# Kernel tuning notes

Measured on AMD Instinct MI355X. Metric: run time of the kernel, lower is better.

Reference implementation:

```python
import jax, jax.numpy as jnp
import numpy as np

N_NODES = 100000
N_EDGES = 1600000
IN_DIM = 128
OUT_DIM = 128
N_HEADS = 4


def setup_inputs() -> dict:
    key = jax.random.key(0)
    k1, k2, k3, k4, k5 = jax.random.split(key, 5)
    h = jax.random.normal(k1, (N_NODES, IN_DIM), dtype=jnp.float32)
    src = jax.random.randint(k2, (N_EDGES,), 0, N_NODES, dtype=jnp.int32)
    dst = jax.random.randint(k3, (N_EDGES,), 0, N_NODES, dtype=jnp.int32)
    s = 1.0 / np.sqrt(IN_DIM)
    W_self = jax.random.normal(k4, (N_HEADS, IN_DIM, OUT_DIM), dtype=jnp.float32) * s
    W_neigh = jax.random.normal(k5, (N_HEADS, IN_DIM, OUT_DIM), dtype=jnp.float32) * s
    b = jnp.zeros((N_HEADS, OUT_DIM), dtype=jnp.float32)
    return {"h": h, "src": src, "dst": dst, "W_self": W_self, "W_neigh": W_neigh, "b": b}


def reference(h, src, dst, W_self, W_neigh, b):
    # Mean neighbor aggregation (shared across heads: SAGEConv 'mean' aggregates
    # raw features, then applies per-head linear layers).
    neigh_sum = jax.ops.segment_sum(h[src], dst, num_segments=N_NODES)   # [N, d_in]
    deg = jax.ops.segment_sum(jnp.ones_like(src, dtype=h.dtype), dst,
                              num_segments=N_NODES)                      # [N]
    h_neigh = neigh_sum / jnp.maximum(deg, 1.0)[:, None]                  # [N, d_in]

    # Per-head: fc_self(h_dst) + fc_neigh(h_neigh) + bias -> [H, N, d_out]
    out = (jnp.einsum('nd,hdo->hno', h, W_self)
           + jnp.einsum('nd,hdo->hno', h_neigh, W_neigh)
           + b[:, None, :])
    # merge='mean': average heads
    return jnp.mean(out, axis=0)  # [N, d_out]
```

## Files before the change

kernel.cpp:

```cpp
#include <hip/hip_runtime.h>

#define N_NODES 100000
#define N_EDGES 1600000
#define DIM 128
#define NH 4

#define NPB 512
#define NB 196
#define CAP 12288
#define BCHUNK 8192
#define BEPT 32
#define NBLK ((N_EDGES + BCHUNK - 1) / BCHUNK)

typedef __attribute__((ext_vector_type(8))) short bf16x8;
typedef __attribute__((ext_vector_type(4))) float f32x4;
typedef __attribute__((ext_vector_type(8))) unsigned short u16x8;

#define B_BCUR   0u
#define B_ROWOFF 4096u
#define B_BBASE  404096u
#define B_CSR    405504u
#define B_WPACK  6805504u
#define B_BAVG   6871040u
#define B_HB     6871552u
#define NEED_BF16 32869376ull

__device__ inline unsigned short f2bf(float x) {
    union { float f; unsigned u; } v; v.f = x;
    unsigned r = v.u + 0x7fffu + ((v.u >> 16) & 1u);
    return (unsigned short)(r >> 16);
}

template <bool BF>
__global__ __launch_bounds__(256) void prep_kernel(
    const float* __restrict__ h, unsigned short* __restrict__ hb,
    const float* __restrict__ Ws, const float* __restrict__ Wn,
    const float* __restrict__ b, unsigned short* __restrict__ wpack,
    float* __restrict__ bavg, int* __restrict__ bcur) {
    const int t = threadIdx.x;
    if (blockIdx.x == 0) bcur[t] = t * CAP;
    int i = blockIdx.x * 256 + t;
    if (i < DIM * DIM) {
        float s = 0.f, n = 0.f;
#pragma unroll
        for (int hh = 0; hh < NH; ++hh) {
            s += Ws[hh * DIM * DIM + i];
            n += Wn[hh * DIM * DIM + i];
        }
        s *= 0.25f; n *= 0.25f;
        int k = i >> 7, o = i & 127;
        int nt = o >> 4, lanelo = o & 15;
        int ks = k >> 5, lanehi = (k & 31) >> 3, e = k & 7;
        int pos = (((nt * 4 + ks) * 64) + lanehi * 16 + lanelo) * 8 + e;
        wpack[pos] = f2bf(s);
        wpack[16384 + pos] = f2bf(n);
    }
    if (i < DIM) {
        float bb = 0.f;
#pragma unroll
        for (int hh = 0; hh < NH; ++hh) bb += b[hh * DIM + i];
        bavg[i] = 0.25f * bb;
    }
    if (BF) {
        const float4* p = reinterpret_cast<const float4*>(h) + (size_t)i * 2;
        float4 a = p[0], c = p[1];
        u16x8 r;
        r[0] = f2bf(a.x); r[1] = f2bf(a.y); r[2] = f2bf(a.z); r[3] = f2bf(a.w);
        r[4] = f2bf(c.x); r[5] = f2bf(c.y); r[6] = f2bf(c.z); r[7] = f2bf(c.w);
        reinterpret_cast<u16x8*>(hb)[i] = r;
    }
}

__global__ __launch_bounds__(256) void bucket_scatter_kernel(const int* __restrict__ src,
                                                             const int* __restrict__ dst,
                                                             int* __restrict__ bcur,
                                                             int* __restrict__ ebuf) {
    __shared__ int stage[BCHUNK];
    __shared__ unsigned char bkt[BCHUNK];
    __shared__ int lc[256], lbase[256], lpos[256];
    int t = threadIdx.x;
    lc[t] = 0;
    lpos[t] = 0;
    __syncthreads();
    int e0 = blockIdx.x * BCHUNK;
#pragma unroll 4
    for (int j = 0; j < BEPT; ++j) {
        int e = e0 + j * 256 + t;
        if (e < N_EDGES) {
            int d = dst[e];
            stage[j * 256 + t] = (src[e] << 9) | (d & (NPB - 1));
            bkt[j * 256 + t] = (unsigned char)(d >> 9);
            atomicAdd(&lc[d >> 9], 1);
        }
    }
    __syncthreads();
    if (lc[t]) lbase[t] = atomicAdd(&bcur[t], lc[t]);
    __syncthreads();
#pragma unroll 4
    for (int j = 0; j < BEPT; ++j) {
        int e = e0 + j * 256 + t;
        if (e < N_EDGES) {
            int bb = bkt[j * 256 + t];
            int o = atomicAdd(&lpos[bb], 1);
            ebuf[lbase[bb] + o] = stage[j * 256 + t];
        }
    }
}

__global__ __launch_bounds__(256) void bucket_scan_kernel(const int* __restrict__ bcur,
                                                          int* __restrict__ bbase) {
    __shared__ int s[256];
    int t = threadIdx.x;
    int v = bcur[t] - t * CAP;
    s[t] = v;
    __syncthreads();
    for (int off = 1; off < 256; off <<= 1) {
        int add = (t >= off) ? s[t - off] : 0;
        __syncthreads();
        s[t] += add;
        __syncthreads();
    }
    bbase[t] = s[t] - v;
}

__global__ __launch_bounds__(256) void csr_build_kernel(const int* __restrict__ bcur,
                                                        const int* __restrict__ bbase,
                                                        const int* __restrict__ ebuf,
                                                        int* __restrict__ rowoff,
                                                        int* __restrict__ csr) {
    __shared__ int h[NPB], off[NPB], cur[NPB], ss[256];
    int b = blockIdx.x, t = threadIdx.x;
    int cnt = bcur[b] - b * CAP;
    int ibase = b * CAP;
    int obase = bbase[b];
    h[t] = 0; h[t + 256] = 0;
    cur[t] = 0; cur[t + 256] = 0;
    __syncthreads();
    for (int i = t; i < cnt; i += 256) atomicAdd(&h[ebuf[ibase + i] & (NPB - 1)], 1);
    __syncthreads();
    int e0 = h[2 * t], e1 = h[2 * t + 1];
    ss[t] = e0 + e1;
    __syncthreads();
    for (int o = 1; o < 256; o <<= 1) {
        int add = (t >= o) ? ss[t - o] : 0;
        __syncthreads();
        ss[t] += add;
        __syncthreads();
    }
    int ex = ss[t] - (e0 + e1);
    off[2 * t] = ex;
    off[2 * t + 1] = ex + e0;
    __syncthreads();
    int n0 = b * NPB;
#pragma unroll
    for (int k = 0; k < 2; ++k) {
        int s2 = 2 * t + k;
        int n = n0 + s2;
        int dg = (k == 0) ? e0 : e1;
        if (n < N_NODES) rowoff[n] = ((obase + off[s2]) << 9) | min(dg, 511);
    }
    for (int i = t; i < cnt; i += 256) {
        int p = ebuf[ibase + i];
        int nl = p & (NPB - 1);
        int o = atomicAdd(&cur[nl], 1);
        csr[obase + off[nl] + o] = p >> 9;
    }
}

template <bool BF>
__global__ __launch_bounds__(256) void gather_mean_kernel(
    const float* __restrict__ h, const unsigned short* __restrict__ hb,
    const int* __restrict__ rowoff, const int* __restrict__ csr,
    float* __restrict__ out) {
    int node = blockIdx.x * 4 + (threadIdx.x >> 6);
    int lane = threadIdx.x & 63;
    int g = lane >> 4;
    int c = lane & 15;
    int w = rowoff[node];
    int lo = w >> 9;
    int dg = w & 511;
    int hi = lo + dg;
    float a0 = 0.f, a1 = 0.f, a2 = 0.f, a3 = 0.f;
    float a4 = 0.f, a5 = 0.f, a6 = 0.f, a7 = 0.f;
    if (BF) {
        int k = lo + g;
        for (; k + 4 < hi; k += 8) {
            int s0 = csr[k], s1 = csr[k + 4];
            uint4 v = *reinterpret_cast<const uint4*>(hb + (size_t)s0 * DIM + c * 8);
            uint4 ww = *reinterpret_cast<const uint4*>(hb + (size_t)s1 * DIM + c * 8);
            a0 += __uint_as_float(v.x << 16) + __uint_as_float(ww.x << 16);
            a1 += __uint_as_float(v.x & 0xffff0000u) + __uint_as_float(ww.x & 0xffff0000u);
            a2 += __uint_as_float(v.y << 16) + __uint_as_float(ww.y << 16);
            a3 += __uint_as_float(v.y & 0xffff0000u) + __uint_as_float(ww.y & 0xffff0000u);
            a4 += __uint_as_float(v.z << 16) + __uint_as_float(ww.z << 16);
            a5 += __uint_as_float(v.z & 0xffff0000u) + __uint_as_float(ww.z & 0xffff0000u);
            a6 += __uint_as_float(v.w << 16) + __uint_as_float(ww.w << 16);
            a7 += __uint_as_float(v.w & 0xffff0000u) + __uint_as_float(ww.w & 0xffff0000u);
        }
        if (k < hi) {
            uint4 v = *reinterpret_cast<const uint4*>(hb + (size_t)csr[k] * DIM + c * 8);
            a0 += __uint_as_float(v.x << 16);
            a1 += __uint_as_float(v.x & 0xffff0000u);
            a2 += __uint_as_float(v.y << 16);
            a3 += __uint_as_float(v.y & 0xffff0000u);
            a4 += __uint_as_float(v.z << 16);
            a5 += __uint_as_float(v.z & 0xffff0000u);
            a6 += __uint_as_float(v.w << 16);
            a7 += __uint_as_float(v.w & 0xffff0000u);
        }
    } else {
        for (int k = lo + g; k < hi; k += 4) {
            int s = csr[k];
            const float4* p = reinterpret_cast<const float4*>(h + (size_t)s * DIM + c * 8);
            float4 x = p[0], y = p[1];
            a0 += x.x; a1 += x.y; a2 += x.z; a3 += x.w;
            a4 += y.x; a5 += y.y; a6 += y.z; a7 += y.w;
        }
    }
    a0 += __shfl_xor(a0, 16, 64); a0 += __shfl_xor(a0, 32, 64);
    a1 += __shfl_xor(a1, 16, 64); a1 += __shfl_xor(a1, 32, 64);
    a2 += __shfl_xor(a2, 16, 64); a2 += __shfl_xor(a2, 32, 64);
    a3 += __shfl_xor(a3, 16, 64); a3 += __shfl_xor(a3, 32, 64);
    a4 += __shfl_xor(a4, 16, 64); a4 += __shfl_xor(a4, 32, 64);
    a5 += __shfl_xor(a5, 16, 64); a5 += __shfl_xor(a5, 32, 64);
    a6 += __shfl_xor(a6, 16, 64); a6 += __shfl_xor(a6, 32, 64);
    a7 += __shfl_xor(a7, 16, 64); a7 += __shfl_xor(a7, 32, 64);
    float inv = 1.0f / (float)max(dg, 1);
    if (g == 0) {
        if (BF) {
            u16x8 r;
            r[0] = f2bf(a0 * inv); r[1] = f2bf(a1 * inv);
            r[2] = f2bf(a2 * inv); r[3] = f2bf(a3 * inv);
            r[4] = f2bf(a4 * inv); r[5] = f2bf(a5 * inv);
            r[6] = f2bf(a6 * inv); r[7] = f2bf(a7 * inv);
            *reinterpret_cast<u16x8*>(reinterpret_cast<unsigned short*>(out) +
                                      (size_t)node * 256 + c * 8) = r;
        } else {
            float4 r0, r1;
            r0.x = a0 * inv; r0.y = a1 * inv; r0.z = a2 * inv; r0.w = a3 * inv;
            r1.x = a4 * inv; r1.y = a5 * inv; r1.z = a6 * inv; r1.w = a7 * inv;
            float4* q = reinterpret_cast<float4*>(out + (size_t)node * DIM + c * 8);
            q[0] = r0;
            q[1] = r1;
        }
    }
}

template <bool BF>
__global__ __launch_bounds__(256) void mfma_gemm_kernel(
    const float* __restrict__ h, const unsigned short* __restrict__ hb,
    float* __restrict__ out, const unsigned short* __restrict__ wpack,
    const float* __restrict__ bavg) {
    const int lane = threadIdx.x & 63;
    const int wid = threadIdx.x >> 6;
    const int node_base = blockIdx.x * 64 + wid * 16;
    const int row = node_base + (lane & 15);
    const int rowc = min(row, N_NODES - 1);
    const int khi = lane >> 4;

    f32x4 acc[8] = {};
    const unsigned short* wn_p = wpack + 16384;

#pragma unroll
    for (int ks = 0; ks < 4; ++ks) {
        const int k0 = ks * 32 + khi * 8;
        bf16x8 ha, na;
        if (BF) {
            ha = *reinterpret_cast<const bf16x8*>(hb + (size_t)rowc * DIM + k0);
            na = *reinterpret_cast<const bf16x8*>(
                reinterpret_cast<const unsigned short*>(out) + (size_t)rowc * 256 + k0);
        } else {
            const float4* hp = reinterpret_cast<const float4*>(h + (size_t)rowc * DIM + k0);
            float4 x = hp[0], y = hp[1];
            ha[0] = (short)f2bf(x.x); ha[1] = (short)f2bf(x.y);
            ha[2] = (short)f2bf(x.z); ha[3] = (short)f2bf(x.w);
            ha[4] = (short)f2bf(y.x); ha[5] = (short)f2bf(y.y);
            ha[6] = (short)f2bf(y.z); ha[7] = (short)f2bf(y.w);
            const float4* np0 = reinterpret_cast<const float4*>(out + (size_t)rowc * DIM + k0);
            float4 u = np0[0], v = np0[1];
            na[0] = (short)f2bf(u.x); na[1] = (short)f2bf(u.y);
            na[2] = (short)f2bf(u.z); na[3] = (short)f2bf(u.w);
            na[4] = (short)f2bf(v.x); na[5] = (short)f2bf(v.y);
            na[6] = (short)f2bf(v.z); na[7] = (short)f2bf(v.w);
        }

#pragma unroll
        for (int nt = 0; nt < 8; ++nt) {
            bf16x8 bs = *reinterpret_cast<const bf16x8*>(wpack + (size_t)(((nt * 4 + ks) * 64 + lane) * 8));
            acc[nt] = __builtin_amdgcn_mfma_f32_16x16x32_bf16(ha, bs, acc[nt], 0, 0, 0);
            bf16x8 bn = *reinterpret_cast<const bf16x8*>(wn_p + (size_t)(((nt * 4 + ks) * 64 + lane) * 8));
            acc[nt] = __builtin_amdgcn_mfma_f32_16x16x32_bf16(na, bn, acc[nt], 0, 0, 0);
        }
    }

    const int r0 = node_base + khi * 4;
#pragma unroll
    for (int nt = 0; nt < 8; ++nt) {
        int o = nt * 16 + (lane & 15);
        float bb = bavg[o];
#pragma unroll
        for (int r = 0; r < 4; ++r) {
            int nr = r0 + r;
            if (nr < N_NODES) out[(size_t)nr * DIM + o] = acc[nt][r] + bb;
        }
    }
}

extern "C" void kernel_launch(void* const* d_in, const int* in_sizes, int n_in,
                              void* d_out, int out_size, void* d_ws, size_t ws_size,
                              hipStream_t stream) {
    const float* h  = (const float*)d_in[0];
    const int* src  = (const int*)d_in[1];
    const int* dst  = (const int*)d_in[2];
    const float* Ws = (const float*)d_in[3];
    const float* Wn = (const float*)d_in[4];
    const float* b  = (const float*)d_in[5];
    float* out = (float*)d_out;

    char* ws = (char*)d_ws;
    int* bcur   = (int*)(ws + B_BCUR);
    int* rowoff = (int*)(ws + B_ROWOFF);
    int* bbase  = (int*)(ws + B_BBASE);
    int* csr    = (int*)(ws + B_CSR);
    unsigned short* wpack = (unsigned short*)(ws + B_WPACK);
    float* bavg = (float*)(ws + B_BAVG);
    unsigned short* hb = (unsigned short*)(ws + B_HB);
    int* ebuf   = (int*)d_out;

    const bool bf = (ws_size >= NEED_BF16);

    if (bf)
        prep_kernel<true><<<(N_NODES * DIM / 8) / 256, 256, 0, stream>>>(h, hb, Ws, Wn, b, wpack, bavg, bcur);
    else
        prep_kernel<false><<<64, 256, 0, stream>>>(h, hb, Ws, Wn, b, wpack, bavg, bcur);
    bucket_scatter_kernel<<<NBLK, 256, 0, stream>>>(src, dst, bcur, ebuf);
    bucket_scan_kernel<<<1, 256, 0, stream>>>(bcur, bbase);
    csr_build_kernel<<<NB, 256, 0, stream>>>(bcur, bbase, ebuf, rowoff, csr);
    if (bf)
        gather_mean_kernel<true><<<N_NODES / 4, 256, 0, stream>>>(h, hb, rowoff, csr, out);
    else
        gather_mean_kernel<false><<<N_NODES / 4, 256, 0, stream>>>(h, hb, rowoff, csr, out);
    const int gemm_blocks = (N_NODES + 63) / 64;
    if (bf)
        mfma_gemm_kernel<true><<<gemm_blocks, 256, 0, stream>>>(h, hb, out, wpack, bavg);
    else
        mfma_gemm_kernel<false><<<gemm_blocks, 256, 0, stream>>>(h, hb, out, wpack, bavg);
}
```

Before: 151.8 us.

## Fuse bucket scatter with prep, fold bucket scan into CSR build

Merges the edge bucket-scatter and the weight/feature bf16 prep into one launch, with block IDs split between the two roles. The separate single-block scan is removed: each CSR-build block recomputes the 256-bucket prefix sum itself, and bucket counters are now zeroed with a memset. Block size goes to 512 threads, so CSR build does one node per thread. This cuts two kernel launches and their serialization gaps, in exchange for a redundant per-block scan and a larger block shape.

```diff
diff --git a/kernel.cpp b/kernel.cpp
--- a/kernel.cpp
+++ b/kernel.cpp
@@ -9,8 +9,11 @@
 #define NB 196
 #define CAP 12288
 #define BCHUNK 8192
-#define BEPT 32
-#define NBLK ((N_EDGES + BCHUNK - 1) / BCHUNK)
+#define SPT 512
+#define BEPT (BCHUNK / SPT)
+#define NBLK 196
+#define NCHUNK (N_NODES * DIM / 8)
+#define CVT_BLKS (NCHUNK / SPT)
 
 typedef __attribute__((ext_vector_type(8))) short bf16x8;
 typedef __attribute__((ext_vector_type(4))) float f32x4;
@@ -18,7 +21,6 @@
 
 #define B_BCUR   0u
 #define B_ROWOFF 4096u
-#define B_BBASE  404096u
 #define B_CSR    405504u
 #define B_WPACK  6805504u
 #define B_BAVG   6871040u
@@ -32,134 +34,115 @@
 }
 
 template <bool BF>
-__global__ __launch_bounds__(256) void prep_kernel(
+__global__ __launch_bounds__(SPT) void scatter_prep_kernel(
+    const int* __restrict__ src, const int* __restrict__ dst,
+    int* __restrict__ bcur, int* __restrict__ ebuf,
     const float* __restrict__ h, unsigned short* __restrict__ hb,
     const float* __restrict__ Ws, const float* __restrict__ Wn,
     const float* __restrict__ b, unsigned short* __restrict__ wpack,
-    float* __restrict__ bavg, int* __restrict__ bcur) {
+    float* __restrict__ bavg) {
     const int t = threadIdx.x;
-    if (blockIdx.x == 0) bcur[t] = t * CAP;
-    int i = blockIdx.x * 256 + t;
-    if (i < DIM * DIM) {
-        float s = 0.f, n = 0.f;
+    if (blockIdx.x >= NBLK) {
+        const int pb = blockIdx.x - NBLK;
+        const int i = pb * SPT + t;
+        if (i < DIM * DIM) {
+            float s = 0.f, n = 0.f;
 #pragma unroll
         for (int hh = 0; hh < NH; ++hh) {
-            s += Ws[hh * DIM * DIM + i];
-            n += Wn[hh * DIM * DIM + i];
-        }
-        s *= 0.25f; n *= 0.25f;
-        int k = i >> 7, o = i & 127;
-        int nt = o >> 4, lanelo = o & 15;
-        int ks = k >> 5, lanehi = (k & 31) >> 3, e = k & 7;
-        int pos = (((nt * 4 + ks) * 64) + lanehi * 16 + lanelo) * 8 + e;
-        wpack[pos] = f2bf(s);
-        wpack[16384 + pos] = f2bf(n);
-    }
-    if (i < DIM) {
-        float bb = 0.f;
-#pragma unroll
-        for (int hh = 0; hh < NH; ++hh) bb += b[hh * DIM + i];
-        bavg[i] = 0.25f * bb;
-    }
-    if (BF) {
-        const float4* p = reinterpret_cast<const float4*>(h) + (size_t)i * 2;
-        float4 a = p[0], c = p[1];
-        u16x8 r;
-        r[0] = f2bf(a.x); r[1] = f2bf(a.y); r[2] = f2bf(a.z); r[3] = f2bf(a.w);
-        r[4] = f2bf(c.x); r[5] = f2bf(c.y); r[6] = f2bf(c.z); r[7] = f2bf(c.w);
-        reinterpret_cast<u16x8*>(hb)[i] = r;
-    }
-}
-
-__global__ __launch_bounds__(256) void bucket_scatter_kernel(const int* __restrict__ src,
-                                                             const int* __restrict__ dst,
-                                                             int* __restrict__ bcur,
-                                                             int* __restrict__ ebuf) {
+                s += Ws[hh * DIM * DIM + i];
+                n += Wn[hh * DIM * DIM + i];
+            }
+            s *= 0.25f; n *= 0.25f;
+            int k = i >> 7, o = i & 127;
+            int nt = o >> 4, lanelo = o & 15;
+            int ks = k >> 5, lanehi = (k & 31) >> 3, e = k & 7;
+            int pos = (((nt * 4 + ks) * 64) + lanehi * 16 + lanelo) * 8 + e;
+            wpack[pos] = f2bf(s);
+            wpack[16384 + pos] = f2bf(n);
+        }
+        if (i < DIM) {
+            float bb = 0.f;
+#pragma unroll
+            for (int hh = 0; hh < NH; ++hh) bb += b[hh * DIM + i];
+            bavg[i] = 0.25f * bb;
+        }
+        if (BF && i < NCHUNK) {
+            const float4* p = reinterpret_cast<const float4*>(h) + (size_t)i * 2;
+            float4 a = p[0], c = p[1];
+            u16x8 r;
+            r[0] = f2bf(a.x); r[1] = f2bf(a.y); r[2] = f2bf(a.z); r[3] = f2bf(a.w);
+            r[4] = f2bf(c.x); r[5] = f2bf(c.y); r[6] = f2bf(c.z); r[7] = f2bf(c.w);
+            reinterpret_cast<u16x8*>(hb)[i] = r;
+        }
+        return;
+    }
     __shared__ int stage[BCHUNK];
     __shared__ unsigned char bkt[BCHUNK];
     __shared__ int lc[256], lbase[256], lpos[256];
-    int t = threadIdx.x;
-    lc[t] = 0;
-    lpos[t] = 0;
+    if (t < 256) { lc[t] = 0; lpos[t] = 0; }
     __syncthreads();
     int e0 = blockIdx.x * BCHUNK;
 #pragma unroll 4
     for (int j = 0; j < BEPT; ++j) {
-        int e = e0 + j * 256 + t;
+        int e = e0 + j * SPT + t;
         if (e < N_EDGES) {
             int d = dst[e];
-            stage[j * 256 + t] = (src[e] << 9) | (d & (NPB - 1));
-            bkt[j * 256 + t] = (unsigned char)(d >> 9);
+            stage[j * SPT + t] = (src[e] << 9) | (d & (NPB - 1));
+            bkt[j * SPT + t] = (unsigned char)(d >> 9);
             atomicAdd(&lc[d >> 9], 1);
         }
     }
     __syncthreads();
-    if (lc[t]) lbase[t] = atomicAdd(&bcur[t], lc[t]);
+    if (t < 256 && lc[t]) lbase[t] = t * CAP + atomicAdd(&bcur[t], lc[t]);
     __syncthreads();
 #pragma unroll 4
     for (int j = 0; j < BEPT; ++j) {
-        int e = e0 + j * 256 + t;
+        int e = e0 + j * SPT + t;
         if (e < N_EDGES) {
-            int bb = bkt[j * 256 + t];
+            int bb = bkt[j * SPT + t];
             int o = atomicAdd(&lpos[bb], 1);
-            ebuf[lbase[bb] + o] = stage[j * 256 + t];
-        }
-    }
-}
-
-__global__ __launch_bounds__(256) void bucket_scan_kernel(const int* __restrict__ bcur,
-                                                          int* __restrict__ bbase) {
-    __shared__ int s[256];
-    int t = threadIdx.x;
-    int v = bcur[t] - t * CAP;
-    s[t] = v;
-    __syncthreads();
-    for (int off = 1; off < 256; off <<= 1) {
-        int add = (t >= off) ? s[t - off] : 0;
-        __syncthreads();
-        s[t] += add;
-        __syncthreads();
-    }
-    bbase[t] = s[t] - v;
-}
-
-__global__ __launch_bounds__(256) void csr_build_kernel(const int* __restrict__ bcur,
-                                                        const int* __restrict__ bbase,
+            ebuf[lbase[bb] + o] = stage[j * SPT + t];
+        }
+    }
+}
+
+__global__ __launch_bounds__(SPT) void csr_build_kernel(const int* __restrict__ bcur,
                                                         const int* __restrict__ ebuf,
                                                         int* __restrict__ rowoff,
                                                         int* __restrict__ csr) {
-    __shared__ int h[NPB], off[NPB], cur[NPB], ss[256];
-    int b = blockIdx.x, t = threadIdx.x;
-    int cnt = bcur[b] - b * CAP;
-    int ibase = b * CAP;
-    int obase = bbase[b];
-    h[t] = 0; h[t + 256] = 0;
-    cur[t] = 0; cur[t + 256] = 0;
-    __syncthreads();
-    for (int i = t; i < cnt; i += 256) atomicAdd(&h[ebuf[ibase + i] & (NPB - 1)], 1);
-    __syncthreads();
-    int e0 = h[2 * t], e1 = h[2 * t + 1];
-    ss[t] = e0 + e1;
+    __shared__ int sh[256];
+    __shared__ int hh[NPB], off[NPB], cur[NPB], ss2[NPB];
+    const int b = blockIdx.x, t = threadIdx.x;
+    const int cnt = bcur[b];
+    const int ibase = b * CAP;
+    if (t < 256) sh[t] = bcur[t];
     __syncthreads();
     for (int o = 1; o < 256; o <<= 1) {
-        int add = (t >= o) ? ss[t - o] : 0;
+        int add = (t < 256 && t >= o) ? sh[t - o] : 0;
         __syncthreads();
-        ss[t] += add;
+        if (t < 256) sh[t] += add;
         __syncthreads();
     }
-    int ex = ss[t] - (e0 + e1);
-    off[2 * t] = ex;
-    off[2 * t + 1] = ex + e0;
-    __syncthreads();
-    int n0 = b * NPB;
-#pragma unroll
-    for (int k = 0; k < 2; ++k) {
-        int s2 = 2 * t + k;
-        int n = n0 + s2;
-        int dg = (k == 0) ? e0 : e1;
-        if (n < N_NODES) rowoff[n] = ((obase + off[s2]) << 9) | min(dg, 511);
-    }
-    for (int i = t; i < cnt; i += 256) {
+    const int obase = sh[b] - cnt;
+    hh[t] = 0;
+    cur[t] = 0;
+    __syncthreads();
+    for (int i = t; i < cnt; i += SPT) atomicAdd(&hh[ebuf[ibase + i] & (NPB - 1)], 1);
+    __syncthreads();
+    const int myc = hh[t];
+    ss2[t] = myc;
+    __syncthreads();
+    for (int o = 1; o < NPB; o <<= 1) {
+        int add = (t >= o) ? ss2[t - o] : 0;
+        __syncthreads();
+        ss2[t] += add;
+        __syncthreads();
+    }
+    off[t] = ss2[t] - myc;
+    __syncthreads();
+    const int n = b * NPB + t;
+    if (n < N_NODES) rowoff[n] = ((obase + off[t]) << 9) | min(myc, 511);
+    for (int i = t; i < cnt; i += SPT) {
         int p = ebuf[ibase + i];
         int nl = p & (NPB - 1);
         int o = atomicAdd(&cur[nl], 1);
@@ -172,14 +155,12 @@
     const float* __restrict__ h, const unsigned short* __restrict__ hb,
     const int* __restrict__ rowoff, const int* __restrict__ csr,
     float* __restrict__ out) {
-    int node = blockIdx.x * 4 + (threadIdx.x >> 6);
-    int lane = threadIdx.x & 63;
-    int g = lane >> 4;
-    int c = lane & 15;
-    int w = rowoff[node];
-    int lo = w >> 9;
-    int dg = w & 511;
-    int hi = lo + dg;
+    const int node = blockIdx.x * 4 + (threadIdx.x >> 6);
+    const int lane = threadIdx.x & 63;
+    const int g = lane >> 4;
+    const int c = lane & 15;
+    const int w = rowoff[node];
+    const int lo = w >> 9, dg = w & 511, hi = lo + dg;
     float a0 = 0.f, a1 = 0.f, a2 = 0.f, a3 = 0.f;
     float a4 = 0.f, a5 = 0.f, a6 = 0.f, a7 = 0.f;
     if (BF) {
@@ -187,15 +168,15 @@
         for (; k + 4 < hi; k += 8) {
             int s0 = csr[k], s1 = csr[k + 4];
             uint4 v = *reinterpret_cast<const uint4*>(hb + (size_t)s0 * DIM + c * 8);
-            uint4 ww = *reinterpret_cast<const uint4*>(hb + (size_t)s1 * DIM + c * 8);
-            a0 += __uint_as_float(v.x << 16) + __uint_as_float(ww.x << 16);
-            a1 += __uint_as_float(v.x & 0xffff0000u) + __uint_as_float(ww.x & 0xffff0000u);
-            a2 += __uint_as_float(v.y << 16) + __uint_as_float(ww.y << 16);
-            a3 += __uint_as_float(v.y & 0xffff0000u) + __uint_as_float(ww.y & 0xffff0000u);
-            a4 += __uint_as_float(v.z << 16) + __uint_as_float(ww.z << 16);
-            a5 += __uint_as_float(v.z & 0xffff0000u) + __uint_as_float(ww.z & 0xffff0000u);
-            a6 += __uint_as_float(v.w << 16) + __uint_as_float(ww.w << 16);
-            a7 += __uint_as_float(v.w & 0xffff0000u) + __uint_as_float(ww.w & 0xffff0000u);
+            uint4 u = *reinterpret_cast<const uint4*>(hb + (size_t)s1 * DIM + c * 8);
+            a0 += __uint_as_float(v.x << 16) + __uint_as_float(u.x << 16);
+            a1 += __uint_as_float(v.x & 0xffff0000u) + __uint_as_float(u.x & 0xffff0000u);
+            a2 += __uint_as_float(v.y << 16) + __uint_as_float(u.y << 16);
+            a3 += __uint_as_float(v.y & 0xffff0000u) + __uint_as_float(u.y & 0xffff0000u);
+            a4 += __uint_as_float(v.z << 16) + __uint_as_float(u.z << 16);
+            a5 += __uint_as_float(v.z & 0xffff0000u) + __uint_as_float(u.z & 0xffff0000u);
+            a6 += __uint_as_float(v.w << 16) + __uint_as_float(u.w << 16);
+            a7 += __uint_as_float(v.w & 0xffff0000u) + __uint_as_float(u.w & 0xffff0000u);
         }
         if (k < hi) {
             uint4 v = *reinterpret_cast<const uint4*>(hb + (size_t)csr[k] * DIM + c * 8);
@@ -210,8 +191,7 @@
         }
     } else {
         for (int k = lo + g; k < hi; k += 4) {
-            int s = csr[k];
-            const float4* p = reinterpret_cast<const float4*>(h + (size_t)s * DIM + c * 8);
+            const float4* p = reinterpret_cast<const float4*>(h + (size_t)csr[k] * DIM + c * 8);
             float4 x = p[0], y = p[1];
             a0 += x.x; a1 += x.y; a2 += x.z; a3 += x.w;
             a4 += y.x; a5 += y.y; a6 += y.z; a7 += y.w;
@@ -228,13 +208,13 @@
     float inv = 1.0f / (float)max(dg, 1);
     if (g == 0) {
         if (BF) {
-            u16x8 r;
-            r[0] = f2bf(a0 * inv); r[1] = f2bf(a1 * inv);
-            r[2] = f2bf(a2 * inv); r[3] = f2bf(a3 * inv);
-            r[4] = f2bf(a4 * inv); r[5] = f2bf(a5 * inv);
-            r[6] = f2bf(a6 * inv); r[7] = f2bf(a7 * inv);
+            u16x8 rr;
+            rr[0] = f2bf(a0 * inv); rr[1] = f2bf(a1 * inv);
+            rr[2] = f2bf(a2 * inv); rr[3] = f2bf(a3 * inv);
+            rr[4] = f2bf(a4 * inv); rr[5] = f2bf(a5 * inv);
+            rr[6] = f2bf(a6 * inv); rr[7] = f2bf(a7 * inv);
             *reinterpret_cast<u16x8*>(reinterpret_cast<unsigned short*>(out) +
-                                      (size_t)node * 256 + c * 8) = r;
+                                      (size_t)node * 256 + c * 8) = rr;
         } else {
             float4 r0, r1;
             r0.x = a0 * inv; r0.y = a1 * inv; r0.z = a2 * inv; r0.w = a3 * inv;
@@ -254,8 +234,7 @@
     const int lane = threadIdx.x & 63;
     const int wid = threadIdx.x >> 6;
     const int node_base = blockIdx.x * 64 + wid * 16;
-    const int row = node_base + (lane & 15);
-    const int rowc = min(row, N_NODES - 1);
+    const int rowc = min(node_base + (lane & 15), N_NODES - 1);
     const int khi = lane >> 4;
 
     f32x4 acc[8] = {};
@@ -320,7 +299,6 @@
     char* ws = (char*)d_ws;
     int* bcur   = (int*)(ws + B_BCUR);
     int* rowoff = (int*)(ws + B_ROWOFF);
-    int* bbase  = (int*)(ws + B_BBASE);
     int* csr    = (int*)(ws + B_CSR);
     unsigned short* wpack = (unsigned short*)(ws + B_WPACK);
     float* bavg = (float*)(ws + B_BAVG);
@@ -329,13 +307,15 @@
 
     const bool bf = (ws_size >= NEED_BF16);
 
+    hipMemsetAsync(bcur, 0, 256 * sizeof(int), stream);
+
     if (bf)
-        prep_kernel<true><<<(N_NODES * DIM / 8) / 256, 256, 0, stream>>>(h, hb, Ws, Wn, b, wpack, bavg, bcur);
+        scatter_prep_kernel<true><<<NBLK + CVT_BLKS, SPT, 0, stream>>>(
+            src, dst, bcur, ebuf, h, hb, Ws, Wn, b, wpack, bavg);
     else
-        prep_kernel<false><<<64, 256, 0, stream>>>(h, hb, Ws, Wn, b, wpack, bavg, bcur);
-    bucket_scatter_kernel<<<NBLK, 256, 0, stream>>>(src, dst, bcur, ebuf);
-    bucket_scan_kernel<<<1, 256, 0, stream>>>(bcur, bbase);
-    csr_build_kernel<<<NB, 256, 0, stream>>>(bcur, bbase, ebuf, rowoff, csr);
+        scatter_prep_kernel<false><<<NBLK + 32, SPT, 0, stream>>>(
+            src, dst, bcur, ebuf, h, hb, Ws, Wn, b, wpack, bavg);
+    csr_build_kernel<<<NB, SPT, 0, stream>>>(bcur, ebuf, rowoff, csr);
     if (bf)
         gather_mean_kernel<true><<<N_NODES / 4, 256, 0, stream>>>(h, hb, rowoff, csr, out);
     else
```

Result: faster. 139.1 us (-8.4%).
